# Kernel tuning notes

Hardware: AMD Instinct MI355X
Metric: run time of the kernel (lower is better)

The kernel has to match this reference:

```python
import jax, jax.numpy as jnp
import numpy as np

COST_CLASS, COST_OBJECTNESS, COST_GIOU, COST_CENTER = 1.0, 0.5, 2.0, 1.0
B, Q, G, C = 32, 4096, 32, 128


def setup_inputs() -> dict:
    key = jax.random.key(0)
    ks = jax.random.split(key, 6)
    return {
        "sem_cls_prob": jax.random.uniform(ks[0], (B, Q, C), jnp.float32),
        "objectness_prob": jax.random.uniform(ks[1], (B, Q), jnp.float32),
        "center_dist": jax.random.uniform(ks[2], (B, Q, G), jnp.float32),
        "gious": jax.random.uniform(ks[3], (B, Q, G), jnp.float32) * 2.0 - 1.0,  # gIoU in [-1,1]
        "gt_box_sem_cls_label": jax.random.randint(ks[4], (B, G), 0, C).astype(jnp.int64),
        "nactual_gt": jax.random.randint(ks[5], (B,), 1, G + 1).astype(jnp.int64),
    }


def _lsa(Cmat):
    """Jonker-Volgenant shortest augmenting path Hungarian.
    Cmat: [n, m] float64 with n <= m. Returns p: [m+1] int64, p[j] = row matched
    to column j (or -1), index m is the virtual start column. Equivalent to
    scipy.optimize.linear_sum_assignment on Cmat (modulo ties)."""
    n, m = Cmat.shape
    u = np.zeros(n, np.float64)
    v = np.zeros(m + 1, np.float64)
    p = np.full(m + 1, -1, np.int64)
    way = np.zeros(m, np.int64)
    for i in range(n):
        p[m] = i
        j0 = m
        minv = np.full(m, np.inf)
        used = np.zeros(m + 1, bool)
        while True:
            used[j0] = True
            i0 = p[j0]
            cur = Cmat[i0] - u[i0] - v[:m]            # vectorized Dijkstra relaxation
            better = (~used[:m]) & (cur < minv)
            minv = np.where(better, cur, minv)
            way = np.where(better, j0, way)
            mv = np.where(used[:m], np.inf, minv)
            j1 = int(np.argmin(mv))
            delta = mv[j1]
            rows = p[used]                            # matched rows of used cols (distinct)
            u[rows] += delta
            v[used] -= delta
            minv = np.where(used[:m], minv, minv - delta)
            j0 = j1
            if p[j0] == -1:
                break
        while j0 != m:                                # augment along the path
            j1 = way[j0]
            p[j0] = p[j1]
            j0 = j1
    return p


def hungarian_assign(final_cost, nactual_gt):
    """final_cost: np [B,Q,G]; emulates the per-batch scipy loop of the module."""
    Bn, Qn, _ = final_cost.shape
    per_prop = np.zeros((Bn, Qn), np.int64)
    mask = np.zeros((Bn, Qn), np.float32)
    for b in range(Bn):
        ng = int(nactual_gt[b])
        if ng > 0:
            p = _lsa(final_cost[b, :, :ng].T.astype(np.float64))  # [ng, Q]
            cols = np.nonzero(p[:Qn] >= 0)[0]
            per_prop[b, cols] = p[cols]
            mask[b, cols] = 1.0
    return per_prop, mask


def build_cost(sem_cls_prob, objectness_prob, center_dist, gious, gt_box_sem_cls_label):
    Bn, Qn, _ = sem_cls_prob.shape
    Gn = gt_box_sem_cls_label.shape[1]
    idx = jnp.broadcast_to(gt_box_sem_cls_label[:, None, :], (Bn, Qn, Gn))
    class_mat = -jnp.take_along_axis(sem_cls_prob, idx, axis=2)        # [B,Q,G]
    return (COST_CLASS * class_mat
            - COST_OBJECTNESS * objectness_prob[:, :, None]
            + COST_CENTER * center_dist
            - COST_GIOU * gious)


def reference(sem_cls_prob, objectness_prob, center_dist, gious, gt_box_sem_cls_label, nactual_gt):
    final_cost = build_cost(sem_cls_prob, objectness_prob, center_dist, gious, gt_box_sem_cls_label)
    cost_np = np.asarray(jax.device_get(final_cost))
    per_prop, mask = hungarian_assign(cost_np, np.asarray(jax.device_get(nactual_gt)))
    return jnp.asarray(per_prop), jnp.asarray(mask)
```

## Files before the change

kernel.cpp:

```cpp
#include <hip/hip_runtime.h>
#include <math.h>

#define NB   32
#define BQ   4096
#define GMAX 32
#define NC   128
#define BS   512
#define CPT  (BQ / BS)
#define NWAVE (BS / 64)

#define TQ   32
#define BBS  256
#define NTILE (BQ / TQ)

#define COST_BYTES ((size_t)NB * GMAX * BQ * 4)

__launch_bounds__(BBS)
__global__ void build_cost_kernel(const float* __restrict__ sem,
                                  const float* __restrict__ objp,
                                  const float* __restrict__ cent,
                                  const float* __restrict__ giou,
                                  const int*   __restrict__ labels,
                                  const int*   __restrict__ nact,
                                  float* __restrict__ cost,
                                  unsigned long long* __restrict__ pmin)
{
    const int b  = blockIdx.y;
    const int qt = blockIdx.x;
    const int q0 = qt * TQ;
    const int tid = threadIdx.x;

    __shared__ float cent_sh[TQ][GMAX + 1];
    __shared__ float giou_sh[TQ][GMAX + 1];
    __shared__ int lab_sh[GMAX];

    if (tid < GMAX) lab_sh[tid] = labels[b * GMAX + tid];
    const int ng = nact[b];

    {
        const float4* centb = (const float4*)(cent + ((size_t)b * BQ + q0) * GMAX);
        const float4* gioub = (const float4*)(giou + ((size_t)b * BQ + q0) * GMAX);
        int r = tid;
        float4 cv = centb[r];
        float4 gv = gioub[r];
        int e = r * 4;
        int qq = e >> 5;
        int ii = e & (GMAX - 1);
        cent_sh[qq][ii]     = cv.x;
        cent_sh[qq][ii + 1] = cv.y;
        cent_sh[qq][ii + 2] = cv.z;
        cent_sh[qq][ii + 3] = cv.w;
        giou_sh[qq][ii]     = gv.x;
        giou_sh[qq][ii + 1] = gv.y;
        giou_sh[qq][ii + 2] = gv.z;
        giou_sh[qq][ii + 3] = gv.w;
    }
    __syncthreads();

    const int qi = tid & (TQ - 1);
    const int ig = tid >> 5;
    const int q  = q0 + qi;
    const float ho = __fmul_rn(0.5f, objp[b * BQ + q]);
    const float* semrow = sem + ((size_t)b * BQ + q) * NC;

    float pc[4];
#pragma unroll
    for (int k = 0; k < 4; k++) {
        int i = ig + 8 * k;
        if (i < ng) pc[k] = semrow[lab_sh[i]];
    }

#pragma unroll
    for (int k = 0; k < 4; k++) {
        int i = ig + 8 * k;
        if (i >= ng) break;
        float ce = cent_sh[qi][i];
        float gi = giou_sh[qi][i];
        float c = __fsub_rn(__fadd_rn(__fsub_rn(-pc[k], ho), ce),
                            __fmul_rn(2.0f, gi));
        __builtin_nontemporal_store(c, &cost[((size_t)b * GMAX + i) * BQ + q]);

        unsigned cbits = __float_as_uint(c);
        unsigned mono  = (cbits & 0x80000000u) ? ~cbits : (cbits | 0x80000000u);
        unsigned long long key = ((unsigned long long)mono << 32) | (unsigned)q;
#pragma unroll
        for (int off = 16; off >= 1; off >>= 1) {
            unsigned long long ok = __shfl_down(key, off, 32);
            if (ok < key) key = ok;
        }
        if (qi == 0) pmin[((size_t)b * GMAX + i) * NTILE + qt] = key;
    }
}

__launch_bounds__(BS, 1)
__global__ void matcher_kernel(const float* __restrict__ cost,
                               const unsigned long long* __restrict__ pmin,
                               const int*   __restrict__ nact,
                               float* __restrict__ out)
{
    const int b    = blockIdx.x;
    const int tid  = threadIdx.x;
    const int m    = BQ;
    const int wave = tid >> 6;
    const int lane = tid & 63;

    __shared__ __align__(16) short p_lds[BQ + 8];
    __shared__ __align__(16) unsigned short way_lds[BQ];
    __shared__ double u_lds[GMAX];
    __shared__ double   redv[2][NWAVE];
    __shared__ unsigned redpk[2][NWAVE];
    __shared__ int    step_i0[GMAX + 2];
    __shared__ double step_D[GMAX + 2];
    __shared__ float  rmin_v[GMAX];
    __shared__ int    rmin_j[GMAX];
    __shared__ int    unmatched[GMAX];
    __shared__ int    s_nunm;

    {
        int4 mone; mone.x = mone.y = mone.z = mone.w = -1;
        ((int4*)p_lds)[tid] = mone;
        if (tid < 4) ((int*)(p_lds + BQ))[tid] = -1;
    }
    const int ng = nact[b];
    const float* cb = cost + (size_t)b * GMAX * BQ;
    __syncthreads();

    {
        const unsigned long long* pb = pmin + (size_t)b * GMAX * NTILE;
        for (int r = wave; r < ng; r += NWAVE) {
            const unsigned long long* row = pb + (size_t)r * NTILE;
            unsigned long long k0 = row[lane];
            unsigned long long k1 = row[lane + 64];
            unsigned long long key = (k1 < k0) ? k1 : k0;
#pragma unroll
            for (int off = 32; off >= 1; off >>= 1) {
                unsigned long long ok = __shfl_down(key, off, 64);
                if (ok < key) key = ok;
            }
            if (lane == 0) {
                unsigned mono = (unsigned)(key >> 32);
                unsigned bits = (mono & 0x80000000u) ? (mono ^ 0x80000000u) : ~mono;
                rmin_v[r] = __uint_as_float(bits);
                rmin_j[r] = (int)(key & 0xFFFFFFFFu);
            }
        }
    }
    __syncthreads();

    if (tid < ng) u_lds[tid] = (double)rmin_v[tid];
    if (tid == 0) {
        int nu = 0;
        for (int i = 0; i < ng; i++) {
            int j = rmin_j[i];
            if (p_lds[j] < 0) p_lds[j] = (short)i;
            else unmatched[nu++] = i;
        }
        s_nunm = nu;
    }
    __syncthreads();
    const int nunm = s_nunm;

    const double INF = (double)INFINITY;
    const int jbase = tid * CPT;
    const float4* cb4 = (const float4*)cb;

    double v_reg[CPT], minv[CPT], enterD[CPT];
    int way_reg[CPT], p_reg[CPT];
#pragma unroll
    for (int k = 0; k < CPT; k++) { v_reg[k] = 0.0; way_reg[k] = m; enterD[k] = 0.0; }

    for (int t = 0; t < nunm; t++) {
        const int ri = unmatched[t];

        int4 pv = ((const int4*)p_lds)[tid];
        p_reg[0] = (int)(short)(pv.x & 0xFFFF); p_reg[1] = pv.x >> 16;
        p_reg[2] = (int)(short)(pv.y & 0xFFFF); p_reg[3] = pv.y >> 16;
        p_reg[4] = (int)(short)(pv.z & 0xFFFF); p_reg[5] = pv.z >> 16;
        p_reg[6] = (int)(short)(pv.w & 0xFFFF); p_reg[7] = pv.w >> 16;

        const float4* r4 = cb4 + (size_t)ri * (BQ / 4) + tid * 2;
        float4 c0 = r4[0];
        float4 c1 = r4[1];
        double ui0 = u_lds[ri];

#pragma unroll
        for (int k = 0; k < CPT; k++) minv[k] = INF;
        unsigned used_mask = 0;
        int i0 = ri, j0 = m, ns = 0, buf = 0, jfin;
        double D = 0.0;

        while (true) {
            float cf[CPT] = {c0.x, c0.y, c0.z, c0.w, c1.x, c1.y, c1.z, c1.w};

            double bestv = INF;
            unsigned bestpk = ((unsigned)m << 8);
#pragma unroll
            for (int k = 0; k < CPT; k++) {
                bool un = !((used_mask >> k) & 1u);
                double cur = ((double)cf[k] - ui0) - v_reg[k];
                bool better = un && (cur < minv[k]);
                if (better) { minv[k] = cur; way_reg[k] = j0; }
                double mv = un ? minv[k] : INF;
                if (mv < bestv) {
                    bestv = mv;
                    bestpk = (((unsigned)(jbase + k)) << 8) | (unsigned)(p_reg[k] + 1);
                }
            }

#pragma unroll
            for (int off = 32; off >= 1; off >>= 1) {
                double   ov  = __shfl_down(bestv, off, 64);
                unsigned opk = __shfl_down(bestpk, off, 64);
                if (ov < bestv || (ov == bestv && opk < bestpk)) { bestv = ov; bestpk = opk; }
            }
            if (lane == 0) { redv[buf][wave] = bestv; redpk[buf][wave] = bestpk; }
            __syncthreads();

            double delta = redv[buf][0]; unsigned pk = redpk[buf][0];
#pragma unroll
            for (int w = 1; w < NWAVE; w++) {
                double ov = redv[buf][w]; unsigned opk = redpk[buf][w];
                if (ov < delta || (ov == delta && opk < pk)) { delta = ov; pk = opk; }
            }
            const int j1 = (int)(pk >> 8);
            const int pi = (int)(pk & 0xFFu) - 1;

            if (tid == 0) { step_i0[ns] = i0; step_D[ns] = D; }
            D += delta;
            ns++;

            if (pi < 0) { jfin = j1; break; }

            const float4* n4 = cb4 + (size_t)pi * (BQ / 4) + tid * 2;
            c0 = n4[0];
            c1 = n4[1];
            ui0 = u_lds[pi];

#pragma unroll
            for (int k = 0; k < CPT; k++)
                if (!((used_mask >> k) & 1u)) minv[k] -= delta;

            unsigned kk = (unsigned)(j1 - jbase);
            if (kk < CPT) { used_mask |= (1u << kk); enterD[kk] = D; }

            i0 = pi; j0 = j1; buf ^= 1;
        }

#pragma unroll
        for (int k = 0; k < CPT; k++)
            if ((used_mask >> k) & 1u) { v_reg[k] -= (D - enterD[k]); }

        int4 wv;
        wv.x = (way_reg[0] & 0xFFFF) | (way_reg[1] << 16);
        wv.y = (way_reg[2] & 0xFFFF) | (way_reg[3] << 16);
        wv.z = (way_reg[4] & 0xFFFF) | (way_reg[5] << 16);
        wv.w = (way_reg[6] & 0xFFFF) | (way_reg[7] << 16);
        ((int4*)way_lds)[tid] = wv;

        __syncthreads();
        if (tid < ns) u_lds[step_i0[tid]] += D - step_D[tid];
        if (tid == 0) {
            int jc = jfin;
            while (jc != m) {
                int jp = (int)way_lds[jc];
                p_lds[jc] = (jp == m) ? (short)ri : p_lds[jp];
                jc = jp;
            }
        }
        __syncthreads();
    }

#pragma unroll
    for (int k = 0; k < CPT; k++) {
        int j = jbase + k;
        short pj = p_lds[j];
        out[(size_t)b * BQ + j] = (pj >= 0) ? (float)pj : 0.0f;
        out[(size_t)NB * BQ + (size_t)b * BQ + j] = (pj >= 0) ? 1.0f : 0.0f;
    }
}

extern "C" void kernel_launch(void* const* d_in, const int* in_sizes, int n_in,
                              void* d_out, int out_size, void* d_ws, size_t ws_size,
                              hipStream_t stream) {
    const float* sem    = (const float*)d_in[0];
    const float* objp   = (const float*)d_in[1];
    const float* cent   = (const float*)d_in[2];
    const float* giou   = (const float*)d_in[3];
    const int*   labels = (const int*)d_in[4];
    const int*   nact   = (const int*)d_in[5];
    float* out  = (float*)d_out;
    float* cost = (float*)d_ws;
    unsigned long long* pmin =
        (unsigned long long*)((char*)d_ws + COST_BYTES);

    dim3 bgrid(NTILE, NB);
    build_cost_kernel<<<bgrid, BBS, 0, stream>>>(sem, objp, cent, giou,
                                                 labels, nact, cost, pmin);
    matcher_kernel<<<NB, BS, 0, stream>>>(cost, pmin, nact, out);
}
```

Before: 138.8 us.

## Recompute cost rows on the fly in matcher instead of materializing cost matrix

Removes the stored transposed cost matrix. The first kernel now emits only per-tile row minima, and the matcher recomputes each needed cost row directly from sem, center, giou and objectness inputs. This avoids writing and re-reading a 16 MB cost buffer. In exchange, each Dijkstra step in the serial matcher now does strided gathers (stride NC or GMAX floats per column), which is uncoalesced and adds latency to every step.

```diff
diff --git a/kernel.cpp b/kernel.cpp
--- a/kernel.cpp
+++ b/kernel.cpp
@@ -13,17 +13,14 @@
 #define BBS  256
 #define NTILE (BQ / TQ)
 
-#define COST_BYTES ((size_t)NB * GMAX * BQ * 4)
-
 __launch_bounds__(BBS)
-__global__ void build_cost_kernel(const float* __restrict__ sem,
-                                  const float* __restrict__ objp,
-                                  const float* __restrict__ cent,
-                                  const float* __restrict__ giou,
-                                  const int*   __restrict__ labels,
-                                  const int*   __restrict__ nact,
-                                  float* __restrict__ cost,
-                                  unsigned long long* __restrict__ pmin)
+__global__ void build_min_kernel(const float* __restrict__ sem,
+                                 const float* __restrict__ objp,
+                                 const float* __restrict__ cent,
+                                 const float* __restrict__ giou,
+                                 const int*   __restrict__ labels,
+                                 const int*   __restrict__ nact,
+                                 unsigned long long* __restrict__ pmin)
 {
     const int b  = blockIdx.y;
     const int qt = blockIdx.x;
@@ -78,7 +75,6 @@
         float gi = giou_sh[qi][i];
         float c = __fsub_rn(__fadd_rn(__fsub_rn(-pc[k], ho), ce),
                             __fmul_rn(2.0f, gi));
-        __builtin_nontemporal_store(c, &cost[((size_t)b * GMAX + i) * BQ + q]);
 
         unsigned cbits = __float_as_uint(c);
         unsigned mono  = (cbits & 0x80000000u) ? ~cbits : (cbits | 0x80000000u);
@@ -93,7 +89,11 @@
 }
 
 __launch_bounds__(BS, 1)
-__global__ void matcher_kernel(const float* __restrict__ cost,
+__global__ void matcher_kernel(const float* __restrict__ sem,
+                               const float* __restrict__ objp,
+                               const float* __restrict__ cent,
+                               const float* __restrict__ giou,
+                               const int*   __restrict__ labels,
                                const unsigned long long* __restrict__ pmin,
                                const int*   __restrict__ nact,
                                float* __restrict__ out)
@@ -113,6 +113,7 @@
     __shared__ double step_D[GMAX + 2];
     __shared__ float  rmin_v[GMAX];
     __shared__ int    rmin_j[GMAX];
+    __shared__ int    lab_sh[GMAX];
     __shared__ int    unmatched[GMAX];
     __shared__ int    s_nunm;
 
@@ -121,8 +122,8 @@
         ((int4*)p_lds)[tid] = mone;
         if (tid < 4) ((int*)(p_lds + BQ))[tid] = -1;
     }
+    if (tid < GMAX) lab_sh[tid] = labels[b * GMAX + tid];
     const int ng = nact[b];
-    const float* cb = cost + (size_t)b * GMAX * BQ;
     __syncthreads();
 
     {
@@ -162,112 +163,133 @@
 
     const double INF = (double)INFINITY;
     const int jbase = tid * CPT;
-    const float4* cb4 = (const float4*)cb;
-
-    double v_reg[CPT], minv[CPT], enterD[CPT];
-    int way_reg[CPT], p_reg[CPT];
-#pragma unroll
-    for (int k = 0; k < CPT; k++) { v_reg[k] = 0.0; way_reg[k] = m; enterD[k] = 0.0; }
-
-    for (int t = 0; t < nunm; t++) {
-        const int ri = unmatched[t];
-
-        int4 pv = ((const int4*)p_lds)[tid];
-        p_reg[0] = (int)(short)(pv.x & 0xFFFF); p_reg[1] = pv.x >> 16;
-        p_reg[2] = (int)(short)(pv.y & 0xFFFF); p_reg[3] = pv.y >> 16;
-        p_reg[4] = (int)(short)(pv.z & 0xFFFF); p_reg[5] = pv.z >> 16;
-        p_reg[6] = (int)(short)(pv.w & 0xFFFF); p_reg[7] = pv.w >> 16;
-
-        const float4* r4 = cb4 + (size_t)ri * (BQ / 4) + tid * 2;
-        float4 c0 = r4[0];
-        float4 c1 = r4[1];
-        double ui0 = u_lds[ri];
-
-#pragma unroll
-        for (int k = 0; k < CPT; k++) minv[k] = INF;
-        unsigned used_mask = 0;
-        int i0 = ri, j0 = m, ns = 0, buf = 0, jfin;
-        double D = 0.0;
-
-        while (true) {
-            float cf[CPT] = {c0.x, c0.y, c0.z, c0.w, c1.x, c1.y, c1.z, c1.w};
-
-            double bestv = INF;
-            unsigned bestpk = ((unsigned)m << 8);
-#pragma unroll
-            for (int k = 0; k < CPT; k++) {
-                bool un = !((used_mask >> k) & 1u);
-                double cur = ((double)cf[k] - ui0) - v_reg[k];
-                bool better = un && (cur < minv[k]);
-                if (better) { minv[k] = cur; way_reg[k] = j0; }
-                double mv = un ? minv[k] : INF;
-                if (mv < bestv) {
-                    bestv = mv;
-                    bestpk = (((unsigned)(jbase + k)) << 8) | (unsigned)(p_reg[k] + 1);
+
+    if (nunm > 0) {
+        const float* semb  = sem  + (size_t)b * BQ * NC;
+        const float* centb = cent + (size_t)b * BQ * GMAX;
+        const float* gioub = giou + (size_t)b * BQ * GMAX;
+        float ho[CPT];
+        {
+            const float* ob = objp + (size_t)b * BQ + jbase;
+#pragma unroll
+            for (int k = 0; k < CPT; k++) ho[k] = __fmul_rn(0.5f, ob[k]);
+        }
+
+        double v_reg[CPT], minv[CPT], enterD[CPT];
+        int way_reg[CPT], p_reg[CPT];
+#pragma unroll
+        for (int k = 0; k < CPT; k++) { v_reg[k] = 0.0; way_reg[k] = m; enterD[k] = 0.0; }
+
+#define ROWCOMP(i, cf)                                                         \
+        {                                                                      \
+            const int li = lab_sh[i];                                          \
+            _Pragma("unroll")                                                  \
+            for (int k = 0; k < CPT; k++) {                                    \
+                const size_t j = (size_t)(jbase + k);                          \
+                float pcls = semb[j * NC + li];                                \
+                float ce   = centb[j * GMAX + (i)];                            \
+                float gi   = gioub[j * GMAX + (i)];                            \
+                cf[k] = __fsub_rn(__fadd_rn(__fsub_rn(-pcls, ho[k]), ce),      \
+                                  __fmul_rn(2.0f, gi));                        \
+            }                                                                  \
+        }
+
+        for (int t = 0; t < nunm; t++) {
+            const int ri = unmatched[t];
+
+            int4 pv = ((const int4*)p_lds)[tid];
+            p_reg[0] = (int)(short)(pv.x & 0xFFFF); p_reg[1] = pv.x >> 16;
+            p_reg[2] = (int)(short)(pv.y & 0xFFFF); p_reg[3] = pv.y >> 16;
+            p_reg[4] = (int)(short)(pv.z & 0xFFFF); p_reg[5] = pv.z >> 16;
+            p_reg[6] = (int)(short)(pv.w & 0xFFFF); p_reg[7] = pv.w >> 16;
+
+            float cf[CPT];
+            ROWCOMP(ri, cf);
+            double ui0 = u_lds[ri];
+
+#pragma unroll
+            for (int k = 0; k < CPT; k++) minv[k] = INF;
+            unsigned used_mask = 0;
+            int i0 = ri, j0 = m, ns = 0, buf = 0, jfin;
+            double D = 0.0;
+
+            while (true) {
+                double bestv = INF;
+                unsigned bestpk = ((unsigned)m << 8);
+#pragma unroll
+                for (int k = 0; k < CPT; k++) {
+                    bool un = !((used_mask >> k) & 1u);
+                    double cur = ((double)cf[k] - ui0) - v_reg[k];
+                    bool better = un && (cur < minv[k]);
+                    if (better) { minv[k] = cur; way_reg[k] = j0; }
+                    double mv = un ? minv[k] : INF;
+                    if (mv < bestv) {
+                        bestv = mv;
+                        bestpk = (((unsigned)(jbase + k)) << 8) | (unsigned)(p_reg[k] + 1);
+                    }
+                }
+
+#pragma unroll
+                for (int off = 32; off >= 1; off >>= 1) {
+                    double   ov  = __shfl_down(bestv, off, 64);
+                    unsigned opk = __shfl_down(bestpk, off, 64);
+                    if (ov < bestv || (ov == bestv && opk < bestpk)) { bestv = ov; bestpk = opk; }
+                }
+                if (lane == 0) { redv[buf][wave] = bestv; redpk[buf][wave] = bestpk; }
+                __syncthreads();
+
+                double delta = redv[buf][0]; unsigned pk = redpk[buf][0];
+#pragma unroll
+                for (int w = 1; w < NWAVE; w++) {
+                    double ov = redv[buf][w]; unsigned opk = redpk[buf][w];
+                    if (ov < delta || (ov == delta && opk < pk)) { delta = ov; pk = opk; }
+                }
+                const int j1 = (int)(pk >> 8);
+                const int pi = (int)(pk & 0xFFu) - 1;
+
+                if (tid == 0) { step_i0[ns] = i0; step_D[ns] = D; }
+                D += delta;
+                ns++;
+
+                if (pi < 0) { jfin = j1; break; }
+
+                ROWCOMP(pi, cf);
+                ui0 = u_lds[pi];
+
+#pragma unroll
+                for (int k = 0; k < CPT; k++)
+                    if (!((used_mask >> k) & 1u)) minv[k] -= delta;
+
+                unsigned kk = (unsigned)(j1 - jbase);
+                if (kk < CPT) { used_mask |= (1u << kk); enterD[kk] = D; }
+
+                i0 = pi; j0 = j1; buf ^= 1;
+            }
+
+#pragma unroll
+            for (int k = 0; k < CPT; k++)
+                if ((used_mask >> k) & 1u) { v_reg[k] -= (D - enterD[k]); }
+
+            int4 wv;
+            wv.x = (way_reg[0] & 0xFFFF) | (way_reg[1] << 16);
+            wv.y = (way_reg[2] & 0xFFFF) | (way_reg[3] << 16);
+            wv.z = (way_reg[4] & 0xFFFF) | (way_reg[5] << 16);
+            wv.w = (way_reg[6] & 0xFFFF) | (way_reg[7] << 16);
+            ((int4*)way_lds)[tid] = wv;
+
+            __syncthreads();
+            if (tid < ns) u_lds[step_i0[tid]] += D - step_D[tid];
+            if (tid == 0) {
+                int jc = jfin;
+                while (jc != m) {
+                    int jp = (int)way_lds[jc];
+                    p_lds[jc] = (jp == m) ? (short)ri : p_lds[jp];
+                    jc = jp;
                 }
             }
-
-#pragma unroll
-            for (int off = 32; off >= 1; off >>= 1) {
-                double   ov  = __shfl_down(bestv, off, 64);
-                unsigned opk = __shfl_down(bestpk, off, 64);
-                if (ov < bestv || (ov == bestv && opk < bestpk)) { bestv = ov; bestpk = opk; }
-            }
-            if (lane == 0) { redv[buf][wave] = bestv; redpk[buf][wave] = bestpk; }
             __syncthreads();
-
-            double delta = redv[buf][0]; unsigned pk = redpk[buf][0];
-#pragma unroll
-            for (int w = 1; w < NWAVE; w++) {
-                double ov = redv[buf][w]; unsigned opk = redpk[buf][w];
-                if (ov < delta || (ov == delta && opk < pk)) { delta = ov; pk = opk; }
-            }
-            const int j1 = (int)(pk >> 8);
-            const int pi = (int)(pk & 0xFFu) - 1;
-
-            if (tid == 0) { step_i0[ns] = i0; step_D[ns] = D; }
-            D += delta;
-            ns++;
-
-            if (pi < 0) { jfin = j1; break; }
-
-            const float4* n4 = cb4 + (size_t)pi * (BQ / 4) + tid * 2;
-            c0 = n4[0];
-            c1 = n4[1];
-            ui0 = u_lds[pi];
-
-#pragma unroll
-            for (int k = 0; k < CPT; k++)
-                if (!((used_mask >> k) & 1u)) minv[k] -= delta;
-
-            unsigned kk = (unsigned)(j1 - jbase);
-            if (kk < CPT) { used_mask |= (1u << kk); enterD[kk] = D; }
-
-            i0 = pi; j0 = j1; buf ^= 1;
-        }
-
-#pragma unroll
-        for (int k = 0; k < CPT; k++)
-            if ((used_mask >> k) & 1u) { v_reg[k] -= (D - enterD[k]); }
-
-        int4 wv;
-        wv.x = (way_reg[0] & 0xFFFF) | (way_reg[1] << 16);
-        wv.y = (way_reg[2] & 0xFFFF) | (way_reg[3] << 16);
-        wv.z = (way_reg[4] & 0xFFFF) | (way_reg[5] << 16);
-        wv.w = (way_reg[6] & 0xFFFF) | (way_reg[7] << 16);
-        ((int4*)way_lds)[tid] = wv;
-
-        __syncthreads();
-        if (tid < ns) u_lds[step_i0[tid]] += D - step_D[tid];
-        if (tid == 0) {
-            int jc = jfin;
-            while (jc != m) {
-                int jp = (int)way_lds[jc];
-                p_lds[jc] = (jp == m) ? (short)ri : p_lds[jp];
-                jc = jp;
-            }
-        }
-        __syncthreads();
+        }
+#undef ROWCOMP
     }
 
 #pragma unroll
@@ -289,12 +311,11 @@
     const int*   labels = (const int*)d_in[4];
     const int*   nact   = (const int*)d_in[5];
     float* out  = (float*)d_out;
-    float* cost = (float*)d_ws;
-    unsigned long long* pmin =
-        (unsigned long long*)((char*)d_ws + COST_BYTES);
+    unsigned long long* pmin = (unsigned long long*)d_ws;
 
     dim3 bgrid(NTILE, NB);
-    build_cost_kernel<<<bgrid, BBS, 0, stream>>>(sem, objp, cent, giou,
-                                                 labels, nact, cost, pmin);
-    matcher_kernel<<<NB, BS, 0, stream>>>(cost, pmin, nact, out);
+    build_min_kernel<<<bgrid, BBS, 0, stream>>>(sem, objp, cent, giou,
+                                                labels, nact, pmin);
+    matcher_kernel<<<NB, BS, 0, stream>>>(sem, objp, cent, giou, labels,
+                                          pmin, nact, out);
 }
```

After: 160.7 us. 1.16x slower.
